# Kernel tuning notes

Hardware: AMD Instinct MI355X
Metric: run time of the kernel (lower is better)

The kernel has to match this reference:

```python
import jax, jax.numpy as jnp
import numpy as np

N0, N1, N2 = 200000, 50000, 10000
E0, E1 = 800000, 160000
IN_DIM, H1, H2, EMB = 256, 256, 256, 128


def gcn_layer(h_src, src_idx, dst_idx, n_src, n_dst, W, b):
    # DGL GraphConv, norm='both': D_dst^{-1/2} A D_src^{-1/2} X W + b,
    # degrees clamped to min 1 (allow_zero_in_degree=True -> zero rows stay zero).
    ones = jnp.ones(src_idx.shape[0], dtype=h_src.dtype)
    out_deg = jnp.clip(jax.ops.segment_sum(ones, src_idx, num_segments=n_src), 1.0)
    in_deg = jnp.clip(jax.ops.segment_sum(ones, dst_idx, num_segments=n_dst), 1.0)
    # in_dim >= out_dim here, so DGL multiplies by W first then aggregates;
    # result is identical either way.
    h = (h_src * jax.lax.rsqrt(out_deg)[:, None]) @ W          # [n_src, out]
    agg = jax.ops.segment_sum(h[src_idx], dst_idx, num_segments=n_dst)  # [n_dst, out]
    return agg * jax.lax.rsqrt(in_deg)[:, None] + b


def setup_inputs() -> dict:
    key = jax.random.key(0)
    ks = jax.random.split(key, 10)
    h = jax.random.normal(ks[0], (N0, IN_DIM), dtype=jnp.float32)
    src0 = jax.random.randint(ks[1], (E0,), 0, N0, dtype=jnp.int32)
    dst0 = jax.random.randint(ks[2], (E0,), 0, N1, dtype=jnp.int32)
    src1 = jax.random.randint(ks[3], (E1,), 0, N1, dtype=jnp.int32)
    dst1 = jax.random.randint(ks[4], (E1,), 0, N2, dtype=jnp.int32)
    s1 = 1.0 / np.sqrt(IN_DIM)
    s2 = 1.0 / np.sqrt(H1)
    sp = 1.0 / np.sqrt(H2)
    W1 = jax.random.normal(ks[5], (IN_DIM, H1), dtype=jnp.float32) * s1
    W2 = jax.random.normal(ks[6], (H1, H2), dtype=jnp.float32) * s2
    Wp = jax.random.normal(ks[7], (H2, EMB), dtype=jnp.float32) * sp
    b1 = jnp.zeros((H1,), dtype=jnp.float32)
    b2 = jnp.zeros((H2,), dtype=jnp.float32)
    bp = jnp.zeros((EMB,), dtype=jnp.float32)
    return {"h": h, "src0": src0, "dst0": dst0, "src1": src1, "dst1": dst1,
            "W1": W1, "b1": b1, "W2": W2, "b2": b2, "Wp": Wp, "bp": bp}


def reference(h, src0, dst0, src1, dst1, W1, b1, W2, b2, Wp, bp):
    h = gcn_layer(h, src0, dst0, N0, N1, W1, b1)   # [N1, H1]
    h = gcn_layer(h, src1, dst1, N1, N2, W2, b2)   # [N2, H2]
    return h @ Wp + bp                             # [N2, EMB]
```

## Files before the change

kernel.cpp:

```cpp
#include <hip/hip_runtime.h>
#include <cstddef>

#define N0 200000
#define N1 50000
#define N2 10000
#define E0 800000
#define E1 160000

typedef short bf16x8 __attribute__((ext_vector_type(8)));
typedef float f32x4 __attribute__((ext_vector_type(4)));
typedef unsigned short us4 __attribute__((ext_vector_type(4)));

__device__ __forceinline__ unsigned short f2bf(float f) {
    unsigned int u = __float_as_uint(f);
    unsigned int r = (u + 0x7FFF + ((u >> 16) & 1)) >> 16;
    return (unsigned short)r;
}
__device__ __forceinline__ float bf2f(unsigned short s) {
    return __uint_as_float(((unsigned int)s) << 16);
}

__global__ void pack_all(const float* __restrict__ W1, const float* __restrict__ W2,
                         const float* __restrict__ Wp,
                         unsigned short* __restrict__ W1p, unsigned short* __restrict__ W2p,
                         unsigned short* __restrict__ Wpp) {
    int tid = blockIdx.x * 256 + threadIdx.x;
    if (tid >= 320 * 64) return;
    int lane = tid & 63;
    int tile = tid >> 6;
    const float* W; unsigned short* Bp; int N; int lt;
    if (tile < 128)      { W = W1; Bp = W1p; N = 256; lt = tile; }
    else if (tile < 256) { W = W2; Bp = W2p; N = 256; lt = tile - 128; }
    else                 { W = Wp; Bp = Wpp; N = 128; lt = tile - 256; }
    int s  = lt & 7;
    int ct = lt >> 3;
    int col = ct * 16 + (lane & 15);
    int k0  = s * 32 + (lane >> 4) * 8;
    unsigned short* dst = Bp + ((size_t)lt * 64 + lane) * 8;
#pragma unroll
    for (int j = 0; j < 8; j++) dst[j] = f2bf(W[(size_t)(k0 + j) * N + col]);
}

__global__ void count_all(const int* __restrict__ src0, const int* __restrict__ dst0,
                          const int* __restrict__ src1, const int* __restrict__ dst1,
                          int* __restrict__ cnt_out0, int* __restrict__ cnt_in0,
                          int* __restrict__ cnt_out1, int* __restrict__ cnt_in1,
                          int* __restrict__ rank0, int* __restrict__ rank1) {
    int e = blockIdx.x * 256 + threadIdx.x;
    if (e < E0) {
        atomicAdd(&cnt_out0[src0[e]], 1);
        rank0[e] = atomicAdd(&cnt_in0[dst0[e]], 1);
    } else if (e < E0 + E1) {
        int f = e - E0;
        atomicAdd(&cnt_out1[src1[f]], 1);
        rank1[f] = atomicAdd(&cnt_in1[dst1[f]], 1);
    }
}

__global__ void scales_kernel(const int* __restrict__ cnt, float* __restrict__ rs, int n) {
    int i = blockIdx.x * 256 + threadIdx.x;
    if (i < n) rs[i] = rsqrtf((float)max(cnt[i], 1));
}

__global__ __launch_bounds__(1024) void scan2(const int* __restrict__ cnt_in0, int* __restrict__ rowptr0,
                                              const int* __restrict__ cnt_in1, int* __restrict__ rowptr1) {
    const int* cnt = blockIdx.x ? cnt_in1 : cnt_in0;
    int* rowptr    = blockIdx.x ? rowptr1 : rowptr0;
    const int n    = blockIdx.x ? N2 : N1;
    __shared__ int partial[1024];
    const int t = threadIdx.x;
    const int chunk = (n + 1023) / 1024;
    const int begin = t * chunk;
    const int end = min(begin + chunk, n);
    int sum = 0;
    for (int i = begin; i < end; i++) sum += cnt[i];
    partial[t] = sum;
    __syncthreads();
    for (int off = 1; off < 1024; off <<= 1) {
        int v = (t >= off) ? partial[t - off] : 0;
        __syncthreads();
        partial[t] += v;
        __syncthreads();
    }
    int run = partial[t] - sum;
    for (int i = begin; i < end; i++) {
        rowptr[i] = run;
        run += cnt[i];
    }
    if (t == 1023) rowptr[n] = partial[1023];
}

__global__ void fill_all(const int* __restrict__ src0, const int* __restrict__ dst0,
                         const int* __restrict__ src1, const int* __restrict__ dst1,
                         const int* __restrict__ rank0, const int* __restrict__ rank1,
                         const int* __restrict__ rowptr0, const int* __restrict__ rowptr1,
                         int* __restrict__ csr0, int* __restrict__ csr1) {
    int e = blockIdx.x * 256 + threadIdx.x;
    if (e < E0) {
        csr0[rowptr0[dst0[e]] + rank0[e]] = src0[e];
    } else if (e < E0 + E1) {
        int f = e - E0;
        csr1[rowptr1[dst1[f]] + rank1[f]] = src1[f];
    }
}

template <int NCT, bool AF32, bool OBF16>
__global__ __launch_bounds__(256) void gemm_mfma(const void* __restrict__ A_,
                                                 const unsigned short* __restrict__ Bp,
                                                 const float* __restrict__ rs,
                                                 const float* __restrict__ bias,
                                                 void* __restrict__ C_, int M, int N) {
    const int lane = threadIdx.x & 63;
    const int wave = threadIdx.x >> 6;
    const int rowBase = blockIdx.x * 64;
    const int colBase = wave * (NCT * 16);
    const int lm = lane & 15;
    const int quad = lane >> 4;

    f32x4 acc[4][NCT];
#pragma unroll
    for (int rt = 0; rt < 4; rt++)
#pragma unroll
        for (int ct = 0; ct < NCT; ct++) acc[rt][ct] = (f32x4){0.f, 0.f, 0.f, 0.f};

    int rowIdx[4];
#pragma unroll
    for (int rt = 0; rt < 4; rt++) rowIdx[rt] = min(rowBase + rt * 16 + lm, M - 1);

    const float* af32 = (const float*)A_;
    const unsigned short* abf = (const unsigned short*)A_;

#pragma unroll
    for (int s = 0; s < 8; s++) {
        bf16x8 afrag[4];
#pragma unroll
        for (int rt = 0; rt < 4; rt++) {
            if (AF32) {
                const float* p = af32 + (size_t)rowIdx[rt] * 256 + quad * 8 + s * 32;
                float4 x = *(const float4*)p;
                float4 y = *(const float4*)(p + 4);
                union { unsigned short u[8]; bf16x8 v; } af;
                af.u[0] = f2bf(x.x); af.u[1] = f2bf(x.y); af.u[2] = f2bf(x.z); af.u[3] = f2bf(x.w);
                af.u[4] = f2bf(y.x); af.u[5] = f2bf(y.y); af.u[6] = f2bf(y.z); af.u[7] = f2bf(y.w);
                afrag[rt] = af.v;
            } else {
                afrag[rt] = *(const bf16x8*)(abf + (size_t)rowIdx[rt] * 256 + quad * 8 + s * 32);
            }
        }
#pragma unroll
        for (int ct = 0; ct < NCT; ct++) {
            bf16x8 bfrag = *(const bf16x8*)(Bp + (((size_t)(wave * NCT + ct) * 8 + s) * 64 + lane) * 8);
#pragma unroll
            for (int rt = 0; rt < 4; rt++)
                acc[rt][ct] = __builtin_amdgcn_mfma_f32_16x16x32_bf16(afrag[rt], bfrag, acc[rt][ct], 0, 0, 0);
        }
    }

#pragma unroll
    for (int rt = 0; rt < 4; rt++) {
        f32x4 rsv = (f32x4){1.f, 1.f, 1.f, 1.f};
        if (rs) rsv = *(const f32x4*)(rs + rowBase + rt * 16 + quad * 4);
#pragma unroll
        for (int ct = 0; ct < NCT; ct++) {
            int col = colBase + ct * 16 + lm;
            float bv = bias ? bias[col] : 0.0f;
#pragma unroll
            for (int i = 0; i < 4; i++) {
                int row = rowBase + rt * 16 + quad * 4 + i;
                if (row < M) {
                    float v = acc[rt][ct][i] * rsv[i] + bv;
                    if (OBF16) ((unsigned short*)C_)[(size_t)row * N + col] = f2bf(v);
                    else       ((float*)C_)[(size_t)row * N + col] = v;
                }
            }
        }
    }
}

__global__ __launch_bounds__(256) void gather_bf16(const unsigned short* __restrict__ Y,
                                                   const int* __restrict__ rowptr,
                                                   const int* __restrict__ csr,
                                                   const float* __restrict__ rs_dst,
                                                   const float* __restrict__ bias,
                                                   unsigned short* __restrict__ outb, int n_dst) {
    int w    = (blockIdx.x * 256 + threadIdx.x) >> 6;
    int lane = threadIdx.x & 63;
    if (w >= n_dst) return;
    int e   = rowptr[w];
    int end = rowptr[w + 1];
    f32x4 acc = (f32x4){0.f, 0.f, 0.f, 0.f};
    for (; e + 3 < end; e += 4) {
        int s0 = csr[e], s1 = csr[e + 1], s2 = csr[e + 2], s3 = csr[e + 3];
        us4 v0 = *(const us4*)(Y + (size_t)s0 * 256 + lane * 4);
        us4 v1 = *(const us4*)(Y + (size_t)s1 * 256 + lane * 4);
        us4 v2 = *(const us4*)(Y + (size_t)s2 * 256 + lane * 4);
        us4 v3 = *(const us4*)(Y + (size_t)s3 * 256 + lane * 4);
        acc[0] += bf2f(v0[0]) + bf2f(v1[0]) + bf2f(v2[0]) + bf2f(v3[0]);
        acc[1] += bf2f(v0[1]) + bf2f(v1[1]) + bf2f(v2[1]) + bf2f(v3[1]);
        acc[2] += bf2f(v0[2]) + bf2f(v1[2]) + bf2f(v2[2]) + bf2f(v3[2]);
        acc[3] += bf2f(v0[3]) + bf2f(v1[3]) + bf2f(v2[3]) + bf2f(v3[3]);
    }
    for (; e < end; e++) {
        int s0 = csr[e];
        us4 v0 = *(const us4*)(Y + (size_t)s0 * 256 + lane * 4);
        acc[0] += bf2f(v0[0]); acc[1] += bf2f(v0[1]); acc[2] += bf2f(v0[2]); acc[3] += bf2f(v0[3]);
    }
    float sd = rs_dst[w];
    f32x4 b = *(const f32x4*)(bias + lane * 4);
    us4 o;
    o[0] = f2bf(acc[0] * sd + b[0]);
    o[1] = f2bf(acc[1] * sd + b[1]);
    o[2] = f2bf(acc[2] * sd + b[2]);
    o[3] = f2bf(acc[3] * sd + b[3]);
    *(us4*)(outb + (size_t)w * 256 + lane * 4) = o;
}

extern "C" void kernel_launch(void* const* d_in, const int* in_sizes, int n_in,
                              void* d_out, int out_size, void* d_ws, size_t ws_size,
                              hipStream_t stream) {
    const float* h    = (const float*)d_in[0];
    const int*   src0 = (const int*)d_in[1];
    const int*   dst0 = (const int*)d_in[2];
    const int*   src1 = (const int*)d_in[3];
    const int*   dst1 = (const int*)d_in[4];
    const float* W1   = (const float*)d_in[5];
    const float* b1   = (const float*)d_in[6];
    const float* W2   = (const float*)d_in[7];
    const float* b2   = (const float*)d_in[8];
    const float* Wp   = (const float*)d_in[9];
    const float* bp   = (const float*)d_in[10];
    float* out = (float*)d_out;

    int* ib = (int*)d_ws;
    int* cnt_out0 = ib;
    int* cnt_in0  = cnt_out0 + N0;
    int* cnt_out1 = cnt_in0 + N1;
    int* cnt_in1  = cnt_out1 + N1;
    int* rowptr0  = ib + 310000;
    int* rowptr1  = ib + 360001;
    int* csr0     = ib + 370004;
    int* csr1     = ib + 1170004;
    float* fb = (float*)(ib + 1330004);
    float* rs_out0 = fb;
    float* rs_in0  = fb + 200000;
    float* rs_out1 = fb + 250000;
    float* rs_in1  = fb + 300000;
    unsigned short* wpk = (unsigned short*)(fb + 310000);
    unsigned short* W1p = wpk;
    unsigned short* W2p = wpk + 65536;
    unsigned short* Wpp = wpk + 131072;
    unsigned short* R   = wpk + 163840;
    int* rank0 = (int*)R;
    int* rank1 = rank0 + E0;
    unsigned short* Y1  = R;
    unsigned short* Y2  = R;
    unsigned short* h2b = R + (size_t)N1 * 256;
    unsigned short* h1b = R + (size_t)N0 * 256;

    hipMemsetAsync(cnt_out0, 0, (size_t)310000 * sizeof(int), stream);

    pack_all<<<80, 256, 0, stream>>>(W1, W2, Wp, W1p, W2p, Wpp);

    count_all<<<(E0 + E1 + 255) / 256, 256, 0, stream>>>(src0, dst0, src1, dst1,
                                                         cnt_out0, cnt_in0, cnt_out1, cnt_in1,
                                                         rank0, rank1);

    scales_kernel<<<(310000 + 255) / 256, 256, 0, stream>>>(cnt_out0, rs_out0, 310000);

    scan2<<<2, 1024, 0, stream>>>(cnt_in0, rowptr0, cnt_in1, rowptr1);

    fill_all<<<(E0 + E1 + 255) / 256, 256, 0, stream>>>(src0, dst0, src1, dst1,
                                                        rank0, rank1, rowptr0, rowptr1, csr0, csr1);

    gemm_mfma<4, true, true><<<N0 / 64, 256, 0, stream>>>(h, W1p, rs_out0, nullptr, Y1, N0, 256);

    gather_bf16<<<(N1 + 3) / 4, 256, 0, stream>>>(Y1, rowptr0, csr0, rs_in0, b1, h1b, N1);

    gemm_mfma<4, false, true><<<(N1 + 63) / 64, 256, 0, stream>>>(h1b, W2p, rs_out1, nullptr, Y2, N1, 256);

    gather_bf16<<<(N2 + 3) / 4, 256, 0, stream>>>(Y2, rowptr1, csr1, rs_in1, b2, h2b, N2);

    gemm_mfma<2, false, false><<<(N2 + 63) / 64, 256, 0, stream>>>(h2b, Wpp, nullptr, bp, out, N2, 128);
}
```

Before: 730.4 us.

## Remap GEMM waves to row strips and widen gather loads to 16 bytes

The GEMM now gives each wave a 16-row strip across all output columns instead of all 64 rows across a column slice. Each A element is therefore loaded and converted to bf16 once rather than once per wave, while B fragments are re-read by every wave. The gather kernel splits each wave into two halves that process alternating edges with 8-element (16-byte) loads and combines them with a cross-half shuffle. This cuts fp32 A-read redundancy in the big first GEMM and raises bytes per load in the gather, at the cost of more accumulator registers per wave and duplicated B traffic.

New measurement: 709.2 us. -2.9%, faster.

```diff
diff --git a/kernel.cpp b/kernel.cpp
--- a/kernel.cpp
+++ b/kernel.cpp
@@ -9,7 +9,7 @@
 
 typedef short bf16x8 __attribute__((ext_vector_type(8)));
 typedef float f32x4 __attribute__((ext_vector_type(4)));
-typedef unsigned short us4 __attribute__((ext_vector_type(4)));
+typedef unsigned short us8 __attribute__((ext_vector_type(8)));
 
 __device__ __forceinline__ unsigned short f2bf(float f) {
     unsigned int u = __float_as_uint(f);
@@ -104,7 +104,7 @@
     }
 }
 
-template <int NCT, bool AF32, bool OBF16>
+template <int NT, bool AF32, bool OBF16>
 __global__ __launch_bounds__(256) void gemm_mfma(const void* __restrict__ A_,
                                                  const unsigned short* __restrict__ Bp,
                                                  const float* __restrict__ rs,
@@ -112,66 +112,51 @@
                                                  void* __restrict__ C_, int M, int N) {
     const int lane = threadIdx.x & 63;
     const int wave = threadIdx.x >> 6;
-    const int rowBase = blockIdx.x * 64;
-    const int colBase = wave * (NCT * 16);
+    const int rowBase = blockIdx.x * 64 + wave * 16;
     const int lm = lane & 15;
     const int quad = lane >> 4;
 
-    f32x4 acc[4][NCT];
-#pragma unroll
-    for (int rt = 0; rt < 4; rt++)
-#pragma unroll
-        for (int ct = 0; ct < NCT; ct++) acc[rt][ct] = (f32x4){0.f, 0.f, 0.f, 0.f};
-
-    int rowIdx[4];
-#pragma unroll
-    for (int rt = 0; rt < 4; rt++) rowIdx[rt] = min(rowBase + rt * 16 + lm, M - 1);
-
-    const float* af32 = (const float*)A_;
-    const unsigned short* abf = (const unsigned short*)A_;
-
-#pragma unroll
+    f32x4 acc[NT];
+#pragma unroll
+    for (int ct = 0; ct < NT; ct++) acc[ct] = (f32x4){0.f, 0.f, 0.f, 0.f};
+
+    const int rowA = min(rowBase + lm, M - 1);
+    const float* af32 = (const float*)A_ + (size_t)rowA * 256 + quad * 8;
+    const unsigned short* abf = (const unsigned short*)A_ + (size_t)rowA * 256 + quad * 8;
+
+#pragma unroll 2
     for (int s = 0; s < 8; s++) {
-        bf16x8 afrag[4];
-#pragma unroll
-        for (int rt = 0; rt < 4; rt++) {
-            if (AF32) {
-                const float* p = af32 + (size_t)rowIdx[rt] * 256 + quad * 8 + s * 32;
-                float4 x = *(const float4*)p;
-                float4 y = *(const float4*)(p + 4);
-                union { unsigned short u[8]; bf16x8 v; } af;
-                af.u[0] = f2bf(x.x); af.u[1] = f2bf(x.y); af.u[2] = f2bf(x.z); af.u[3] = f2bf(x.w);
-                af.u[4] = f2bf(y.x); af.u[5] = f2bf(y.y); af.u[6] = f2bf(y.z); af.u[7] = f2bf(y.w);
-                afrag[rt] = af.v;
-            } else {
-                afrag[rt] = *(const bf16x8*)(abf + (size_t)rowIdx[rt] * 256 + quad * 8 + s * 32);
-            }
+        bf16x8 afrag;
+        if (AF32) {
+            float4 x = *(const float4*)(af32 + s * 32);
+            float4 y = *(const float4*)(af32 + s * 32 + 4);
+            union { unsigned short u[8]; bf16x8 v; } af;
+            af.u[0] = f2bf(x.x); af.u[1] = f2bf(x.y); af.u[2] = f2bf(x.z); af.u[3] = f2bf(x.w);
+            af.u[4] = f2bf(y.x); af.u[5] = f2bf(y.y); af.u[6] = f2bf(y.z); af.u[7] = f2bf(y.w);
+            afrag = af.v;
+        } else {
+            afrag = *(const bf16x8*)(abf + s * 32);
         }
 #pragma unroll
-        for (int ct = 0; ct < NCT; ct++) {
-            bf16x8 bfrag = *(const bf16x8*)(Bp + (((size_t)(wave * NCT + ct) * 8 + s) * 64 + lane) * 8);
-#pragma unroll
-            for (int rt = 0; rt < 4; rt++)
-                acc[rt][ct] = __builtin_amdgcn_mfma_f32_16x16x32_bf16(afrag[rt], bfrag, acc[rt][ct], 0, 0, 0);
+        for (int ct = 0; ct < NT; ct++) {
+            bf16x8 bfrag = *(const bf16x8*)(Bp + (((size_t)ct * 8 + s) * 64 + lane) * 8);
+            acc[ct] = __builtin_amdgcn_mfma_f32_16x16x32_bf16(afrag, bfrag, acc[ct], 0, 0, 0);
         }
     }
 
-#pragma unroll
-    for (int rt = 0; rt < 4; rt++) {
-        f32x4 rsv = (f32x4){1.f, 1.f, 1.f, 1.f};
-        if (rs) rsv = *(const f32x4*)(rs + rowBase + rt * 16 + quad * 4);
-#pragma unroll
-        for (int ct = 0; ct < NCT; ct++) {
-            int col = colBase + ct * 16 + lm;
-            float bv = bias ? bias[col] : 0.0f;
-#pragma unroll
-            for (int i = 0; i < 4; i++) {
-                int row = rowBase + rt * 16 + quad * 4 + i;
-                if (row < M) {
-                    float v = acc[rt][ct][i] * rsv[i] + bv;
-                    if (OBF16) ((unsigned short*)C_)[(size_t)row * N + col] = f2bf(v);
-                    else       ((float*)C_)[(size_t)row * N + col] = v;
-                }
+    f32x4 rsv = (f32x4){1.f, 1.f, 1.f, 1.f};
+    if (rs) rsv = *(const f32x4*)(rs + rowBase + quad * 4);
+#pragma unroll
+    for (int ct = 0; ct < NT; ct++) {
+        int col = ct * 16 + lm;
+        float bv = bias ? bias[col] : 0.0f;
+#pragma unroll
+        for (int i = 0; i < 4; i++) {
+            int row = rowBase + quad * 4 + i;
+            if (row < M) {
+                float v = acc[ct][i] * rsv[i] + bv;
+                if (OBF16) ((unsigned short*)C_)[(size_t)row * N + col] = f2bf(v);
+                else       ((float*)C_)[(size_t)row * N + col] = v;
             }
         }
     }
@@ -186,33 +171,53 @@
     int w    = (blockIdx.x * 256 + threadIdx.x) >> 6;
     int lane = threadIdx.x & 63;
     if (w >= n_dst) return;
+    int half = lane >> 5;
+    int l32  = lane & 31;
     int e   = rowptr[w];
     int end = rowptr[w + 1];
-    f32x4 acc = (f32x4){0.f, 0.f, 0.f, 0.f};
-    for (; e + 3 < end; e += 4) {
-        int s0 = csr[e], s1 = csr[e + 1], s2 = csr[e + 2], s3 = csr[e + 3];
-        us4 v0 = *(const us4*)(Y + (size_t)s0 * 256 + lane * 4);
-        us4 v1 = *(const us4*)(Y + (size_t)s1 * 256 + lane * 4);
-        us4 v2 = *(const us4*)(Y + (size_t)s2 * 256 + lane * 4);
-        us4 v3 = *(const us4*)(Y + (size_t)s3 * 256 + lane * 4);
-        acc[0] += bf2f(v0[0]) + bf2f(v1[0]) + bf2f(v2[0]) + bf2f(v3[0]);
-        acc[1] += bf2f(v0[1]) + bf2f(v1[1]) + bf2f(v2[1]) + bf2f(v3[1]);
-        acc[2] += bf2f(v0[2]) + bf2f(v1[2]) + bf2f(v2[2]) + bf2f(v3[2]);
-        acc[3] += bf2f(v0[3]) + bf2f(v1[3]) + bf2f(v2[3]) + bf2f(v3[3]);
-    }
-    for (; e < end; e++) {
+    float acc[8] = {0.f, 0.f, 0.f, 0.f, 0.f, 0.f, 0.f, 0.f};
+    for (; e + 7 < end; e += 8) {
+        int s0 = csr[e + half];
+        int s1 = csr[e + 2 + half];
+        int s2 = csr[e + 4 + half];
+        int s3 = csr[e + 6 + half];
+        us8 v0 = *(const us8*)(Y + (size_t)s0 * 256 + l32 * 8);
+        us8 v1 = *(const us8*)(Y + (size_t)s1 * 256 + l32 * 8);
+        us8 v2 = *(const us8*)(Y + (size_t)s2 * 256 + l32 * 8);
+        us8 v3 = *(const us8*)(Y + (size_t)s3 * 256 + l32 * 8);
+#pragma unroll
+        for (int j = 0; j < 8; j++)
+            acc[j] += (bf2f(v0[j]) + bf2f(v1[j])) + (bf2f(v2[j]) + bf2f(v3[j]));
+    }
+    for (; e + 1 < end; e += 2) {
+        int s0 = csr[e + half];
+        us8 v0 = *(const us8*)(Y + (size_t)s0 * 256 + l32 * 8);
+#pragma unroll
+        for (int j = 0; j < 8; j++) acc[j] += bf2f(v0[j]);
+    }
+    if (e < end && half == 0) {
         int s0 = csr[e];
-        us4 v0 = *(const us4*)(Y + (size_t)s0 * 256 + lane * 4);
-        acc[0] += bf2f(v0[0]); acc[1] += bf2f(v0[1]); acc[2] += bf2f(v0[2]); acc[3] += bf2f(v0[3]);
-    }
-    float sd = rs_dst[w];
-    f32x4 b = *(const f32x4*)(bias + lane * 4);
-    us4 o;
-    o[0] = f2bf(acc[0] * sd + b[0]);
-    o[1] = f2bf(acc[1] * sd + b[1]);
-    o[2] = f2bf(acc[2] * sd + b[2]);
-    o[3] = f2bf(acc[3] * sd + b[3]);
-    *(us4*)(outb + (size_t)w * 256 + lane * 4) = o;
+        us8 v0 = *(const us8*)(Y + (size_t)s0 * 256 + l32 * 8);
+#pragma unroll
+        for (int j = 0; j < 8; j++) acc[j] += bf2f(v0[j]);
+    }
+#pragma unroll
+    for (int j = 0; j < 8; j++) acc[j] += __shfl_xor(acc[j], 32);
+    if (half == 0) {
+        float sd = rs_dst[w];
+        f32x4 ba = *(const f32x4*)(bias + l32 * 8);
+        f32x4 bb = *(const f32x4*)(bias + l32 * 8 + 4);
+        us8 o;
+        o[0] = f2bf(acc[0] * sd + ba[0]);
+        o[1] = f2bf(acc[1] * sd + ba[1]);
+        o[2] = f2bf(acc[2] * sd + ba[2]);
+        o[3] = f2bf(acc[3] * sd + ba[3]);
+        o[4] = f2bf(acc[4] * sd + bb[0]);
+        o[5] = f2bf(acc[5] * sd + bb[1]);
+        o[6] = f2bf(acc[6] * sd + bb[2]);
+        o[7] = f2bf(acc[7] * sd + bb[3]);
+        *(us8*)(outb + (size_t)w * 256 + l32 * 8) = o;
+    }
 }
 
 extern "C" void kernel_launch(void* const* d_in, const int* in_sizes, int n_in,
@@ -272,13 +277,13 @@
     fill_all<<<(E0 + E1 + 255) / 256, 256, 0, stream>>>(src0, dst0, src1, dst1,
                                                         rank0, rank1, rowptr0, rowptr1, csr0, csr1);
 
-    gemm_mfma<4, true, true><<<N0 / 64, 256, 0, stream>>>(h, W1p, rs_out0, nullptr, Y1, N0, 256);
+    gemm_mfma<16, true, true><<<N0 / 64, 256, 0, stream>>>(h, W1p, rs_out0, nullptr, Y1, N0, 256);
 
     gather_bf16<<<(N1 + 3) / 4, 256, 0, stream>>>(Y1, rowptr0, csr0, rs_in0, b1, h1b, N1);
 
-    gemm_mfma<4, false, true><<<(N1 + 63) / 64, 256, 0, stream>>>(h1b, W2p, rs_out1, nullptr, Y2, N1, 256);
+    gemm_mfma<16, false, true><<<(N1 + 63) / 64, 256, 0, stream>>>(h1b, W2p, rs_out1, nullptr, Y2, N1, 256);
 
     gather_bf16<<<(N2 + 3) / 4, 256, 0, stream>>>(Y2, rowptr1, csr1, rs_in1, b2, h2b, N2);
 
-    gemm_mfma<2, false, false><<<(N2 + 63) / 64, 256, 0, stream>>>(h2b, Wpp, nullptr, bp, out, N2, 128);
-}
+    gemm_mfma<8, false, false><<<(N2 + 63) / 64, 256, 0, stream>>>(h2b, Wpp, nullptr, bp, out, N2, 128);
+}
```
